# Kernel optimization log

Hardware: AMD Instinct MI355X
Metric: run time of the kernel (lower is better)

Reference implementation:

```python
import jax, jax.numpy as jnp
import numpy as np

NUM_HEADS = 12   # H
NUM_TASKS = 4    # T
TOP_K = 2        # capacity_factor


def setup_inputs() -> dict:
    key = jax.random.key(0)
    ks = jax.random.split(key, 4)
    B, N, C = 2, 4100, 768  # N = NUM_TASKS + M, M = 4096
    x = jax.random.normal(ks[0], (B, N, C), dtype=jnp.float32)
    # torch.nn.Linear weights are [out_features, in_features]; y = x @ W.T
    qs_w = jax.random.normal(ks[1], (NUM_TASKS, C, C), dtype=jnp.float32) * 0.02
    kv_w = jax.random.normal(ks[2], (2 * C, C), dtype=jnp.float32) * 0.02
    experts_w = jax.random.normal(ks[3], (NUM_TASKS, C, C), dtype=jnp.float32) * 0.02
    return {"x": x, "qs_w": qs_w, "kv_w": kv_w, "experts_w": experts_w}


def reference(x, qs_w, kv_w, experts_w):
    B, N, C = x.shape
    T, H, K = NUM_TASKS, NUM_HEADS, TOP_K
    d = C // H
    M = N - T
    scale = d ** -0.5

    feature = x[:, T:, :]                                    # [B,M,C]
    kv = (feature @ kv_w.T).reshape(B, M, 2, H, d)
    k = jnp.transpose(kv[:, :, 0], (0, 2, 1, 3))             # [B,H,M,d]
    v = jnp.transpose(kv[:, :, 1], (0, 2, 1, 3))             # [B,H,M,d]

    # per-task q projections on task tokens (qs_w[t] is [out,in])
    q = jnp.einsum('btc,toc->bto', x[:, :T], qs_w)           # [B,T,C]
    q = q.reshape(B, T, H, d).transpose(0, 2, 1, 3)          # [B,H,T,d]

    attn = jnp.einsum('bhtd,bhmd->bhtm', q, k) * scale       # [B,H,T,M]
    topv, topi = jax.lax.top_k(attn, K)                      # [B,H,T,K]
    topw = jax.nn.softmax(topv, axis=-1)                     # softmax over top-k only

    # scatter softmaxed top-k back into dense [B,H,T,M] (indices unique per row)
    oh = jax.nn.one_hot(topi, M, dtype=x.dtype)              # [B,H,T,K,M]
    attn_topk = jnp.einsum('bhtk,bhtkm->bhtm', topw, oh)
    attn_token = jnp.einsum('bhtm,bhmd->bhtd', attn_topk, v)
    attn_token = attn_token.transpose(0, 2, 1, 3).reshape(B, T, C)   # [B,T,C]

    # gather top-k feature rows per head/task, weight, and scatter back
    fm = feature.reshape(B, M, H, d).transpose(0, 2, 1, 3)   # [B,H,M,d]
    feat_topk = jnp.take_along_axis(fm[:, :, None], topi[..., None], axis=3)  # [B,H,T,K,d]
    feat_topk = feat_topk * topw[..., None]
    # scatter to [B,H,T,M,d], then permute(0,2,3,1,4)+reshape -> [B,T,M,C]
    feat_pad = jnp.einsum('bhtkd,bhtkm->btmhd', feat_topk, oh).reshape(B, T, M, C)

    # per-task experts (no bias); einsum('btnc,btnc->bnc') with ones = sum over t
    feature_output = jnp.einsum('btmc,toc->bmo', feat_pad, experts_w)  # [B,M,C]
    token_output = jnp.einsum('btc,toc->bto', attn_token, experts_w)   # [B,T,C]

    return jnp.concatenate([token_output, feature_output], axis=1)     # [B,N,C]
```

## Files before the change

kernel.cpp:

```cpp
#include <hip/hip_runtime.h>
#include <math.h>

#define B_ 2
#define N_ 4100
#define C_ 768
#define T_ 4
#define H_ 12
#define D_ 64
#define M_ 4096
#define S_ 48
#define KS_ 12
#define KC_ 64
#define NJ_ 16
#define MT_ 128
#define SEG_ 8
#define SCALE 0.125f

__device__ __forceinline__ bool better(float va, int ia, float vb, int ib) {
  return (va > vb) || (va == vb && ia < ib);
}

__device__ __forceinline__ void merge2(float& v1, int& i1, float& v2, int& i2,
                                       float ov1, int oi1, float ov2, int oi2) {
  if (better(ov1, oi1, v1, i1)) {
    float tv; int ti;
    tv = v1; ti = i1; v1 = ov1; i1 = oi1; ov1 = tv; oi1 = ti;
    tv = v2; ti = i2; v2 = ov2; i2 = oi2; ov2 = tv; oi2 = ti;
  }
  if (better(ov1, oi1, v2, i2)) { v2 = ov1; i2 = oi1; }
}

__global__ __launch_bounds__(256) void qk_kernel(const float* __restrict__ x,
    const float* __restrict__ qs_w, const float* __restrict__ kv_w,
    float* __restrict__ qk) {
  const int blk = blockIdx.x;
  const int tid = threadIdx.x;
  const int h = blk % H_;
  const int t = (blk / H_) % T_;
  const int b = blk / S_;
  __shared__ float xs[C_];
  __shared__ float red[256];
  __shared__ float qseg[D_];
  for (int i = tid; i < C_; i += 256) xs[i] = x[((size_t)b * N_ + t) * C_ + i];
  __syncthreads();
  {
    const int j = tid & 63;
    const int pt = tid >> 6;
    const float* wr = qs_w + ((size_t)t * C_ + h * D_ + j) * C_ + pt * 192;
    float a = 0.f;
    for (int c = 0; c < 192; ++c) a += xs[pt * 192 + c] * wr[c];
    red[tid] = a;
  }
  __syncthreads();
  if (tid < 64)
    qseg[tid] = (red[tid] + red[tid + 64] + red[tid + 128] + red[tid + 192]) * SCALE;
  __syncthreads();
  for (int c = tid; c < C_; c += 256) {
    float a = 0.f;
    #pragma unroll 8
    for (int j = 0; j < 64; ++j) a += qseg[j] * kv_w[((size_t)(h * D_ + j)) * C_ + c];
    qk[(size_t)blk * C_ + c] = a;
  }
}

__global__ __launch_bounds__(256, 3) void score_kernel(const float* __restrict__ x,
    const float* __restrict__ qk, float* __restrict__ part) {
  const int bm = blockIdx.x & 31;
  const int b  = blockIdx.x >> 5;
  const int kc = blockIdx.y;
  const int tid = threadIdx.x;

  __shared__ __align__(16) float fbuf[MT_][68];
  __shared__ __align__(16) float qbuf[S_][KC_];

  {
    const char* xb = (const char*)(x + ((size_t)b * N_ + T_ + bm * MT_) * C_ + kc * KC_);
    #pragma unroll
    for (int i = 0; i < 8; ++i) {
      unsigned g = i * 256 + tid;
      unsigned r = g >> 4, j = g & 15;
      *(float4*)&fbuf[r][j * 4] = *(const float4*)(xb + (size_t)r * (C_ * 4) + j * 16);
    }
  }
  {
    const char* qb = (const char*)(qk + (size_t)b * S_ * C_ + kc * KC_);
    #pragma unroll
    for (int i = 0; i < 3; ++i) {
      unsigned g = i * 256 + tid;
      unsigned s = g >> 4, j = g & 15;
      *(float4*)&qbuf[s][j * 4] = *(const float4*)(qb + (size_t)s * (C_ * 4) + j * 16);
    }
  }
  __syncthreads();

  const int w = tid >> 6;
  const int lane = tid & 63;
  const int s0 = w * 12;

  float acc[12][2];
  #pragma unroll
  for (int si = 0; si < 12; ++si) {
    acc[si][0] = 0.f; acc[si][1] = 0.f;
  }

  #pragma unroll 2
  for (int j = 0; j < NJ_; ++j) {
    float4 f0 = *(const float4*)&fbuf[lane     ][j * 4];
    float4 f1 = *(const float4*)&fbuf[lane + 64][j * 4];
    #pragma unroll
    for (int si = 0; si < 12; ++si) {
      float4 q = *(const float4*)&qbuf[s0 + si][j * 4];
      acc[si][0] += f0.x * q.x + f0.y * q.y + f0.z * q.z + f0.w * q.w;
      acc[si][1] += f1.x * q.x + f1.y * q.y + f1.z * q.z + f1.w * q.w;
    }
  }

  const int m0 = bm * MT_;
  #pragma unroll
  for (int si = 0; si < 12; ++si) {
    float* pp = part + (((size_t)kc * B_ + b) * S_ + (s0 + si)) * M_ + m0 + lane;
    pp[0]  = acc[si][0];
    pp[64] = acc[si][1];
  }
}

__global__ __launch_bounds__(256) void reduce_kernel(const float* __restrict__ part,
                                                     float* __restrict__ cand) {
  const int seg = blockIdx.x & 7;
  const int bs = blockIdx.x >> 3;
  const int tid = threadIdx.x;
  const size_t kstride = (size_t)B_ * S_ * M_;
  const float* p0 = part + (size_t)bs * M_ + seg * 512 + tid * 2;
  float a0 = 0.f, a1 = 0.f;
  #pragma unroll
  for (int kc = 0; kc < KS_; ++kc) {
    float2 v = *(const float2*)(p0 + kc * kstride);
    a0 += v.x; a1 += v.y;
  }
  const int mA = seg * 512 + tid * 2;
  float v1, v2; int i1, i2;
  if (better(a0, mA, a1, mA + 1)) { v1 = a0; i1 = mA; v2 = a1; i2 = mA + 1; }
  else                            { v1 = a1; i1 = mA + 1; v2 = a0; i2 = mA; }
  #pragma unroll
  for (int off = 1; off < 64; off <<= 1) {
    float ov1 = __shfl_xor(v1, off);
    int   oi1 = __shfl_xor(i1, off);
    float ov2 = __shfl_xor(v2, off);
    int   oi2 = __shfl_xor(i2, off);
    merge2(v1, i1, v2, i2, ov1, oi1, ov2, oi2);
  }
  __shared__ float cbuf[4][4];
  const int w = tid >> 6, lane = tid & 63;
  if (lane == 0) {
    cbuf[w][0] = v1; ((int*)cbuf[w])[1] = i1;
    cbuf[w][2] = v2; ((int*)cbuf[w])[3] = i2;
  }
  __syncthreads();
  if (tid == 0) {
    for (int ww = 1; ww < 4; ++ww)
      merge2(v1, i1, v2, i2, cbuf[ww][0], ((int*)cbuf[ww])[1],
             cbuf[ww][2], ((int*)cbuf[ww])[3]);
    ((float4*)cand)[blockIdx.x] =
        make_float4(v1, __int_as_float(i1), v2, __int_as_float(i2));
  }
}

__global__ __launch_bounds__(256) void gatherA_kernel(const float* __restrict__ x,
    const float* __restrict__ kv_w, const float* __restrict__ cand,
    float* __restrict__ selws) {
  const int h = blockIdx.x % H_;
  const int b = blockIdx.x / S_;
  const int tid = threadIdx.x;

  __shared__ __align__(16) float fc[C_];
  __shared__ float red[256];
  __shared__ float sel[4];

  if (tid < 8) {
    float4 cv = ((const float4*)cand)[blockIdx.x * 8 + tid];
    float v1 = cv.x, v2 = cv.z;
    int i1 = __float_as_int(cv.y), i2 = __float_as_int(cv.w);
    #pragma unroll
    for (int off = 1; off < 8; off <<= 1) {
      float ov1 = __shfl_xor(v1, off);
      int   oi1 = __shfl_xor(i1, off);
      float ov2 = __shfl_xor(v2, off);
      int   oi2 = __shfl_xor(i2, off);
      merge2(v1, i1, v2, i2, ov1, oi1, ov2, oi2);
    }
    if (tid == 0) {
      float w1 = 1.f / (1.f + expf(v2 - v1));
      ((int*)sel)[0] = i1; ((int*)sel)[1] = i2;
      sel[2] = w1; sel[3] = 1.f - w1;
    }
  }
  __syncthreads();
  const int i1 = ((const int*)sel)[0];
  const int i2 = ((const int*)sel)[1];
  const float w1 = sel[2], w2 = sel[3];

  const float* r0 = x + ((size_t)b * N_ + T_ + i1) * C_;
  const float* r1 = x + ((size_t)b * N_ + T_ + i2) * C_;
  for (int i = tid; i < C_; i += 256)
    fc[i] = w1 * r0[i] + w2 * r1[i];
  __syncthreads();

  {
    const int j = tid & 63, pt = tid >> 6;
    const float4* kr4 = (const float4*)(kv_w + ((size_t)(C_ + h * D_ + j)) * C_ + pt * 192);
    const float4* fc4 = (const float4*)(&fc[pt * 192]);
    float a = 0.f;
    #pragma unroll 8
    for (int c4 = 0; c4 < 48; ++c4) {
      float4 kv = kr4[c4], fv = fc4[c4];
      a += kv.x * fv.x + kv.y * fv.y + kv.z * fv.z + kv.w * fv.w;
    }
    red[tid] = a;
  }
  __syncthreads();
  if (tid < 64)
    selws[(size_t)blockIdx.x * 72 + tid] =
        red[tid] + red[tid + 64] + red[tid + 128] + red[tid + 192];
  else if (tid < 68)
    selws[(size_t)blockIdx.x * 72 + tid] = sel[tid - 64];
}

__global__ __launch_bounds__(256) void scatter_kernel(const float* __restrict__ x,
    const float* __restrict__ experts_w, const float* __restrict__ selws,
    float* __restrict__ out) {
  const int bs = blockIdx.x >> 3, oc = blockIdx.x & 7;
  const int h = bs % H_;
  const int t = (bs / H_) % T_;
  const int b = bs / S_;
  const int tid = threadIdx.x;

  __shared__ __align__(16) float attnh[D_], g0s[D_], g1s[D_];
  __shared__ float psel[4];

  if (tid < 4) psel[tid] = selws[(size_t)bs * 72 + 64 + tid];
  __syncthreads();
  const int i1 = __float_as_int(psel[0]);
  const int i2 = __float_as_int(psel[1]);
  const float w1 = psel[2], w2 = psel[3];

  if (tid < 64) {
    attnh[tid] = selws[(size_t)bs * 72 + tid];
    g0s[tid] = x[((size_t)b * N_ + T_ + i1) * C_ + h * D_ + tid];
    g1s[tid] = x[((size_t)b * N_ + T_ + i2) * C_ + h * D_ + tid];
  }
  __syncthreads();

  if (tid < 96) {
    const int o = oc * 96 + tid;
    const float4* er4 = (const float4*)(experts_w + ((size_t)t * C_ + o) * C_ + h * D_);
    const float4* at4 = (const float4*)attnh;
    const float4* g04 = (const float4*)g0s;
    const float4* g14 = (const float4*)g1s;
    float at = 0.f, a0 = 0.f, a1 = 0.f;
    #pragma unroll
    for (int c4 = 0; c4 < 16; ++c4) {
      float4 e = er4[c4];
      float4 av = at4[c4], v0 = g04[c4], v1 = g14[c4];
      at += e.x * av.x + e.y * av.y + e.z * av.z + e.w * av.w;
      a0 += e.x * v0.x + e.y * v0.y + e.z * v0.z + e.w * v0.w;
      a1 += e.x * v1.x + e.y * v1.y + e.z * v1.z + e.w * v1.w;
    }
    atomicAdd(&out[((size_t)b * N_ + t) * C_ + o], at);
    atomicAdd(&out[((size_t)b * N_ + T_ + i1) * C_ + o], w1 * a0);
    atomicAdd(&out[((size_t)b * N_ + T_ + i2) * C_ + o], w2 * a1);
  }
}

extern "C" void kernel_launch(void* const* d_in, const int* in_sizes, int n_in,
                              void* d_out, int out_size, void* d_ws, size_t ws_size,
                              hipStream_t stream) {
  const float* x         = (const float*)d_in[0];
  const float* qs_w      = (const float*)d_in[1];
  const float* kv_w      = (const float*)d_in[2];
  const float* experts_w = (const float*)d_in[3];
  float* out = (float*)d_out;

  float* ws    = (float*)d_ws;
  float* qk    = ws;
  float* part  = qk + (size_t)B_ * S_ * C_;
  float* cand  = part + (size_t)KS_ * B_ * S_ * M_;
  float* selws = cand + (size_t)B_ * S_ * SEG_ * 4;

  hipLaunchKernelGGL(qk_kernel,      dim3(B_ * S_),        dim3(256), 0, stream, x, qs_w, kv_w, qk);
  hipLaunchKernelGGL(score_kernel,   dim3(B_ * 32, KS_),   dim3(256), 0, stream, x, qk, part);
  hipLaunchKernelGGL(reduce_kernel,  dim3(B_ * S_ * SEG_), dim3(256), 0, stream, part, cand);
  hipLaunchKernelGGL(gatherA_kernel, dim3(B_ * S_),        dim3(256), 0, stream, x, kv_w, cand, selws);
  hipLaunchKernelGGL(scatter_kernel, dim3(B_ * S_ * 8),    dim3(256), 0, stream, x, experts_w, selws, out);
}
```

Before: 137.1 us.

## Double-buffer score kernel shared tiles with register-prefetched K sub-chunks

The score kernel used to load the whole 64-wide K chunk of features and queries into shared memory before computing. It now splits that chunk into four 16-wide sub-chunks and keeps two shared buffers. The next sub-chunk is prefetched into registers while the current one is computed, so global load latency overlaps with FMA work. Shared memory per block also shrinks, which may allow more blocks per CU. In exchange the kernel adds extra __syncthreads barriers on each sub-chunk step and holds more registers for the prefetched values.

```diff
diff --git a/kernel.cpp b/kernel.cpp
--- a/kernel.cpp
+++ b/kernel.cpp
@@ -11,7 +11,6 @@
 #define S_ 48
 #define KS_ 12
 #define KC_ 64
-#define NJ_ 16
 #define MT_ 128
 #define SEG_ 8
 #define SCALE 0.125f
@@ -70,27 +69,26 @@
   const int kc = blockIdx.y;
   const int tid = threadIdx.x;
 
-  __shared__ __align__(16) float fbuf[MT_][68];
-  __shared__ __align__(16) float qbuf[S_][KC_];
-
-  {
-    const char* xb = (const char*)(x + ((size_t)b * N_ + T_ + bm * MT_) * C_ + kc * KC_);
-    #pragma unroll
-    for (int i = 0; i < 8; ++i) {
-      unsigned g = i * 256 + tid;
-      unsigned r = g >> 4, j = g & 15;
-      *(float4*)&fbuf[r][j * 4] = *(const float4*)(xb + (size_t)r * (C_ * 4) + j * 16);
-    }
-  }
-  {
-    const char* qb = (const char*)(qk + (size_t)b * S_ * C_ + kc * KC_);
-    #pragma unroll
-    for (int i = 0; i < 3; ++i) {
-      unsigned g = i * 256 + tid;
-      unsigned s = g >> 4, j = g & 15;
-      *(float4*)&qbuf[s][j * 4] = *(const float4*)(qb + (size_t)s * (C_ * 4) + j * 16);
-    }
-  }
+  __shared__ __align__(16) float fbuf[2][MT_][20];
+  __shared__ __align__(16) float qbuf[2][S_][16];
+
+  const char* xb = (const char*)(x + ((size_t)b * N_ + T_ + bm * MT_) * C_ + kc * KC_);
+  const char* qb = (const char*)(qk + (size_t)b * S_ * C_ + kc * KC_);
+
+  const unsigned fr0 = tid >> 2,          fj0 = tid & 3;
+  const unsigned fr1 = (256 + tid) >> 2,  fj1 = tid & 3;
+  const unsigned qs  = tid >> 2,          qj  = tid & 3;
+
+  float4 fA, fB, qA;
+  fA = *(const float4*)(xb + (size_t)fr0 * (C_ * 4) + (fj0 * 16));
+  fB = *(const float4*)(xb + (size_t)fr1 * (C_ * 4) + (fj1 * 16));
+  if (tid < 192) qA = *(const float4*)(qb + (size_t)qs * (C_ * 4) + (qj * 16));
+  *(float4*)&fbuf[0][fr0][fj0 * 4] = fA;
+  *(float4*)&fbuf[0][fr1][fj1 * 4] = fB;
+  if (tid < 192) *(float4*)&qbuf[0][qs][qj * 4] = qA;
+  fA = *(const float4*)(xb + (size_t)fr0 * (C_ * 4) + (64 + fj0 * 16));
+  fB = *(const float4*)(xb + (size_t)fr1 * (C_ * 4) + (64 + fj1 * 16));
+  if (tid < 192) qA = *(const float4*)(qb + (size_t)qs * (C_ * 4) + (64 + qj * 16));
   __syncthreads();
 
   const int w = tid >> 6;
@@ -103,15 +101,32 @@
     acc[si][0] = 0.f; acc[si][1] = 0.f;
   }
 
-  #pragma unroll 2
-  for (int j = 0; j < NJ_; ++j) {
-    float4 f0 = *(const float4*)&fbuf[lane     ][j * 4];
-    float4 f1 = *(const float4*)&fbuf[lane + 64][j * 4];
+  #pragma unroll
+  for (int h = 0; h < 4; ++h) {
+    const int cb = h & 1;
     #pragma unroll
-    for (int si = 0; si < 12; ++si) {
-      float4 q = *(const float4*)&qbuf[s0 + si][j * 4];
-      acc[si][0] += f0.x * q.x + f0.y * q.y + f0.z * q.z + f0.w * q.w;
-      acc[si][1] += f1.x * q.x + f1.y * q.y + f1.z * q.z + f1.w * q.w;
+    for (int j = 0; j < 4; ++j) {
+      float4 f0 = *(const float4*)&fbuf[cb][lane     ][j * 4];
+      float4 f1 = *(const float4*)&fbuf[cb][lane + 64][j * 4];
+      #pragma unroll
+      for (int si = 0; si < 12; ++si) {
+        float4 q = *(const float4*)&qbuf[cb][s0 + si][j * 4];
+        acc[si][0] += f0.x * q.x + f0.y * q.y + f0.z * q.z + f0.w * q.w;
+        acc[si][1] += f1.x * q.x + f1.y * q.y + f1.z * q.z + f1.w * q.w;
+      }
+    }
+    if (h < 3) {
+      __syncthreads();
+      const int nb = (h + 1) & 1;
+      *(float4*)&fbuf[nb][fr0][fj0 * 4] = fA;
+      *(float4*)&fbuf[nb][fr1][fj1 * 4] = fB;
+      if (tid < 192) *(float4*)&qbuf[nb][qs][qj * 4] = qA;
+      if (h + 2 < 4) {
+        fA = *(const float4*)(xb + (size_t)fr0 * (C_ * 4) + ((h + 2) * 64 + fj0 * 16));
+        fB = *(const float4*)(xb + (size_t)fr1 * (C_ * 4) + ((h + 2) * 64 + fj1 * 16));
+        if (tid < 192) qA = *(const float4*)(qb + (size_t)qs * (C_ * 4) + ((h + 2) * 64 + qj * 16));
+      }
+      __syncthreads();
     }
   }
 
```

New measurement: 525.2 us. 283% more time.

## Split score kernel feature tile into two halves to overlap loads with compute

Applied to the files above, without the earlier changes.

The score kernel now loads its 128x64 feature tile in two 32-column halves. The second half is prefetched into registers while the first half is computed from shared memory, then written to a second smaller buffer. The change also pads the rows differently (36 and 68 floats) to alter the bank layout. It aims to hide global load latency behind the first half's FMAs, at the cost of extra barriers and added register pressure under launch bounds of 3 blocks.

```diff
diff --git a/kernel.cpp b/kernel.cpp
--- a/kernel.cpp
+++ b/kernel.cpp
@@ -11,7 +11,6 @@
 #define S_ 48
 #define KS_ 12
 #define KC_ 64
-#define NJ_ 16
 #define MT_ 128
 #define SEG_ 8
 #define SCALE 0.125f
@@ -70,27 +69,34 @@
   const int kc = blockIdx.y;
   const int tid = threadIdx.x;
 
-  __shared__ __align__(16) float fbuf[MT_][68];
-  __shared__ __align__(16) float qbuf[S_][KC_];
-
+  __shared__ __align__(16) float fbuf[2][MT_][36];
+  __shared__ __align__(16) float qbuf[S_][68];
+
+  const char* xb = (const char*)(x + ((size_t)b * N_ + T_ + bm * MT_) * C_ + kc * KC_);
+  const char* qb = (const char*)(qk + (size_t)b * S_ * C_ + kc * KC_);
+
+  const unsigned fr0 = tid >> 3, fj = tid & 7;
+  const unsigned qs = tid >> 4, qj = tid & 15;
+
+  float4 hA[4];
+  #pragma unroll
+  for (int i = 0; i < 4; ++i)
+    hA[i] = *(const float4*)(xb + (size_t)(fr0 + 32 * i) * (C_ * 4) + fj * 16);
   {
-    const char* xb = (const char*)(x + ((size_t)b * N_ + T_ + bm * MT_) * C_ + kc * KC_);
-    #pragma unroll
-    for (int i = 0; i < 8; ++i) {
-      unsigned g = i * 256 + tid;
-      unsigned r = g >> 4, j = g & 15;
-      *(float4*)&fbuf[r][j * 4] = *(const float4*)(xb + (size_t)r * (C_ * 4) + j * 16);
-    }
-  }
-  {
-    const char* qb = (const char*)(qk + (size_t)b * S_ * C_ + kc * KC_);
-    #pragma unroll
-    for (int i = 0; i < 3; ++i) {
-      unsigned g = i * 256 + tid;
-      unsigned s = g >> 4, j = g & 15;
-      *(float4*)&qbuf[s][j * 4] = *(const float4*)(qb + (size_t)s * (C_ * 4) + j * 16);
-    }
-  }
+    float4 qv[3];
+    #pragma unroll
+    for (int i = 0; i < 3; ++i)
+      qv[i] = *(const float4*)(qb + (size_t)(qs + 16 * i) * (C_ * 4) + qj * 16);
+    #pragma unroll
+    for (int i = 0; i < 4; ++i)
+      *(float4*)&fbuf[0][fr0 + 32 * i][fj * 4] = hA[i];
+    #pragma unroll
+    for (int i = 0; i < 3; ++i)
+      *(float4*)&qbuf[qs + 16 * i][qj * 4] = qv[i];
+  }
+  #pragma unroll
+  for (int i = 0; i < 4; ++i)
+    hA[i] = *(const float4*)(xb + (size_t)(fr0 + 32 * i) * (C_ * 4) + 128 + fj * 16);
   __syncthreads();
 
   const int w = tid >> 6;
@@ -104,12 +110,28 @@
   }
 
   #pragma unroll 2
-  for (int j = 0; j < NJ_; ++j) {
-    float4 f0 = *(const float4*)&fbuf[lane     ][j * 4];
-    float4 f1 = *(const float4*)&fbuf[lane + 64][j * 4];
+  for (int j = 0; j < 8; ++j) {
+    float4 f0 = *(const float4*)&fbuf[0][lane     ][j * 4];
+    float4 f1 = *(const float4*)&fbuf[0][lane + 64][j * 4];
     #pragma unroll
     for (int si = 0; si < 12; ++si) {
       float4 q = *(const float4*)&qbuf[s0 + si][j * 4];
+      acc[si][0] += f0.x * q.x + f0.y * q.y + f0.z * q.z + f0.w * q.w;
+      acc[si][1] += f1.x * q.x + f1.y * q.y + f1.z * q.z + f1.w * q.w;
+    }
+  }
+  __syncthreads();
+  #pragma unroll
+  for (int i = 0; i < 4; ++i)
+    *(float4*)&fbuf[1][fr0 + 32 * i][fj * 4] = hA[i];
+  __syncthreads();
+  #pragma unroll 2
+  for (int j = 0; j < 8; ++j) {
+    float4 f0 = *(const float4*)&fbuf[1][lane     ][j * 4];
+    float4 f1 = *(const float4*)&fbuf[1][lane + 64][j * 4];
+    #pragma unroll
+    for (int si = 0; si < 12; ++si) {
+      float4 q = *(const float4*)&qbuf[s0 + si][32 + j * 4];
       acc[si][0] += f0.x * q.x + f0.y * q.y + f0.z * q.z + f0.w * q.w;
       acc[si][1] += f1.x * q.x + f1.y * q.y + f1.z * q.z + f1.w * q.w;
     }
```

Measured after the change: 143.9 us. 4.9% more time.
